# Performance work log

Hardware: AMD Instinct MI355X
Metric: run time of the kernel (lower is better)

Reference implementation:

```python
import jax, jax.numpy as jnp
import numpy as np

NUM_HEADS = 16

def setup_inputs() -> dict:
    key = jax.random.key(0)
    ks = jax.random.split(key, 7)
    B, Q, K, D = 4, 512, 4096, 1024
    return {
        'query':  jax.random.normal(ks[0], (B, Q, D), dtype=jnp.float32),
        'memory': jax.random.normal(ks[1], (B, K, D), dtype=jnp.float32),
        'bias':   jax.random.normal(ks[2], (B, K), dtype=jnp.float32),
        'Wq': jax.random.normal(ks[3], (D, D), dtype=jnp.float32) * (D ** -0.5),
        'Wk': jax.random.normal(ks[4], (D, D), dtype=jnp.float32) * (D ** -0.5),
        'Wv': jax.random.normal(ks[5], (D, D), dtype=jnp.float32) * (D ** -0.5),
        'Wo': jax.random.normal(ks[6], (D, D), dtype=jnp.float32) * (D ** -0.5),
    }

def reference(query, memory, bias, Wq, Wk, Wv, Wo):
    B, Qn, _ = query.shape
    _, Kn, _ = memory.shape
    H = NUM_HEADS
    E = Wq.shape[1]
    dh = E // H
    scale = dh ** -0.5
    # projections (bias-free linears), split heads: [B, H, len, dh]
    q = (query @ Wq).reshape(B, Qn, H, dh).transpose(0, 2, 1, 3)
    k = (memory @ Wk).reshape(B, Kn, H, dh).transpose(0, 2, 1, 3)
    v = (memory @ Wv).reshape(B, Kn, H, dh).transpose(0, 2, 1, 3)
    scores = jnp.einsum('bhqd,bhkd->bhqk', q, k) * scale
    scores = scores + bias[:, None, None, :]          # additive support bias over K
    weights = jax.nn.softmax(scores, axis=-1)          # dropout p=0.0 -> identity
    out = jnp.einsum('bhqk,bhkd->bhqd', weights, v)
    out = out.transpose(0, 2, 1, 3).reshape(B, Qn, E)
    return out @ Wo
```

## Files before the change

kernel.cpp:

```cpp
#include <hip/hip_runtime.h>

typedef __attribute__((ext_vector_type(8))) short bf16x8;
typedef __attribute__((ext_vector_type(4))) short bf16x4;
typedef __attribute__((ext_vector_type(4))) float f32x4;

#define MFMA32(a,b,c) __builtin_amdgcn_mfma_f32_16x16x32_bf16((a),(b),(c),0,0,0)
#define MFMA16(a,b,c) __builtin_amdgcn_mfma_f32_16x16x16bf16_1k((a),(b),(c),0,0,0)
#define LOG2E 1.44269504f

__device__ __forceinline__ unsigned short f2bf(float f) {
  unsigned int u = __float_as_uint(f);
  u += 0x7fffu + ((u >> 16) & 1u);
  return (unsigned short)(u >> 16);
}

__device__ __forceinline__ void cp16(const void* g, void* l) {
  __builtin_amdgcn_global_load_lds((const __attribute__((address_space(1))) void*)g,
                                   (__attribute__((address_space(3))) void*)l, 16, 0, 0);
}

__global__ void conv_both(const float* __restrict__ q, const float* __restrict__ m,
                          const float* __restrict__ bias,
                          unsigned short* __restrict__ qo, unsigned short* __restrict__ mo,
                          float* __restrict__ bz) {
  int i = blockIdx.x * 256 + threadIdx.x;
  if (i < 524288) {
    float4 v = ((const float4*)q)[i];
    ushort4 o; o.x = f2bf(v.x); o.y = f2bf(v.y); o.z = f2bf(v.z); o.w = f2bf(v.w);
    ((ushort4*)qo)[i] = o;
  } else if (i < 4718592) {
    int j = i - 524288;
    float4 v = ((const float4*)m)[j];
    ushort4 o; o.x = f2bf(v.x); o.y = f2bf(v.y); o.z = f2bf(v.z); o.w = f2bf(v.w);
    ((ushort4*)mo)[j] = o;
  } else {
    int j = i - 4718592;
    float4 v = ((const float4*)bias)[j];
    float4 o;
    o.x = __builtin_fmaf(v.x, LOG2E, -16.f);
    o.y = __builtin_fmaf(v.y, LOG2E, -16.f);
    o.z = __builtin_fmaf(v.z, LOG2E, -16.f);
    o.w = __builtin_fmaf(v.w, LOG2E, -16.f);
    ((float4*)bz)[j] = o;
  }
}

__global__ void transpose4(const float* __restrict__ Wq, const float* __restrict__ Wk,
                           const float* __restrict__ Wv, const float* __restrict__ Wo,
                           unsigned short* __restrict__ dst) {
  __shared__ float t[32][33];
  int z = blockIdx.z;
  const float* W = (z == 0) ? Wq : (z == 1) ? Wk : (z == 2) ? Wv : Wo;
  unsigned short* WT = dst + (size_t)z * 1048576;
  int bx = blockIdx.x * 32, by = blockIdx.y * 32;
  int x = threadIdx.x, y0 = threadIdx.y;
#pragma unroll
  for (int r = 0; r < 4; ++r)
    t[y0 + r * 8][x] = W[(size_t)(by + y0 + r * 8) * 1024 + bx + x];
  __syncthreads();
#pragma unroll
  for (int r = 0; r < 4; ++r)
    WT[(size_t)(bx + y0 + r * 8) * 1024 + by + x] = f2bf(t[x][y0 + r * 8]);
}

__global__ __launch_bounds__(256) void gemm_bt(
    const unsigned short* __restrict__ A, const unsigned short* __restrict__ B,
    float* __restrict__ Cf, unsigned short* __restrict__ Cb,
    int M, int N, int K, float scale)
{
  __shared__ __attribute__((aligned(16))) unsigned short lds[8192];
  int w = threadIdx.x >> 6, lane = threadIdx.x & 63;
  int lh = lane & 15, q4 = lane >> 4;
  int tm = blockIdx.y * 128, tn = blockIdx.x * 128;
  int wm = (w & 1) * 64, wn = (w >> 1) * 64;

  f32x4 acc[4][4] = {};

  for (int k0 = 0; k0 < K; k0 += 32) {
#pragma unroll
    for (int i = 0; i < 2; ++i) {
      int c = w * 2 + i;
      int o = c * 1024 + lane * 16;
      int row = o >> 6;
      int colu = (o & 63) >> 1;
      cp16(A + (size_t)(tm + row) * K + k0 + colu, lds + c * 512);
      cp16(B + (size_t)(tn + row) * K + k0 + colu, lds + 4096 + c * 512);
    }
    __syncthreads();
    bf16x8 afr[4], bfr[4];
#pragma unroll
    for (int r = 0; r < 4; ++r)
      afr[r] = *(const bf16x8*)(lds + (wm + r * 16 + lh) * 32 + q4 * 8);
#pragma unroll
    for (int c = 0; c < 4; ++c)
      bfr[c] = *(const bf16x8*)(lds + 4096 + (wn + c * 16 + lh) * 32 + q4 * 8);
#pragma unroll
    for (int r = 0; r < 4; ++r)
#pragma unroll
      for (int c = 0; c < 4; ++c)
        acc[r][c] = MFMA32(afr[r], bfr[c], acc[r][c]);
    __syncthreads();
  }

#pragma unroll
  for (int r = 0; r < 4; ++r)
#pragma unroll
    for (int c = 0; c < 4; ++c)
#pragma unroll
      for (int e = 0; e < 4; ++e) {
        int row = tm + wm + r * 16 + q4 * 4 + e;
        int col = tn + wn + c * 16 + lh;
        if (Cb) Cb[(size_t)row * N + col] = f2bf(acc[r][c][e] * scale);
        else    Cf[(size_t)row * N + col] = acc[r][c][e] * scale;
      }
}

__global__ __launch_bounds__(256) void gemm_bt64(
    const unsigned short* __restrict__ A, const unsigned short* __restrict__ B,
    float* __restrict__ Cf, unsigned short* __restrict__ Cb,
    int M, int N, int K, float scale)
{
  __shared__ __attribute__((aligned(16))) unsigned short lds[6144];
  int w = threadIdx.x >> 6, lane = threadIdx.x & 63;
  int lh = lane & 15, q4 = lane >> 4;
  int tm = blockIdx.y * 128, tn = blockIdx.x * 64;
  int wm = (w & 1) * 64, wn = (w >> 1) * 32;

  f32x4 acc[4][2] = {};

  for (int k0 = 0; k0 < K; k0 += 32) {
#pragma unroll
    for (int i = 0; i < 2; ++i) {
      int c = w * 2 + i;
      int o = c * 1024 + lane * 16;
      int row = o >> 6, colu = (o & 63) >> 1;
      cp16(A + (size_t)(tm + row) * K + k0 + colu, lds + c * 512);
    }
    {
      int o = w * 1024 + lane * 16;
      int row = o >> 6, colu = (o & 63) >> 1;
      cp16(B + (size_t)(tn + row) * K + k0 + colu, lds + 4096 + w * 512);
    }
    __syncthreads();
    bf16x8 afr[4], bfr[2];
#pragma unroll
    for (int r = 0; r < 4; ++r)
      afr[r] = *(const bf16x8*)(lds + (wm + r * 16 + lh) * 32 + q4 * 8);
#pragma unroll
    for (int c = 0; c < 2; ++c)
      bfr[c] = *(const bf16x8*)(lds + 4096 + (wn + c * 16 + lh) * 32 + q4 * 8);
#pragma unroll
    for (int r = 0; r < 4; ++r)
#pragma unroll
      for (int c = 0; c < 2; ++c)
        acc[r][c] = MFMA32(afr[r], bfr[c], acc[r][c]);
    __syncthreads();
  }

#pragma unroll
  for (int r = 0; r < 4; ++r)
#pragma unroll
    for (int c = 0; c < 2; ++c)
#pragma unroll
      for (int e = 0; e < 4; ++e) {
        int row = tm + wm + r * 16 + q4 * 4 + e;
        int col = tn + wn + c * 16 + lh;
        if (Cb) Cb[(size_t)row * N + col] = f2bf(acc[r][c][e] * scale);
        else    Cf[(size_t)row * N + col] = acc[r][c][e] * scale;
      }
}

__global__ __launch_bounds__(256) void attn_kernel(
    const unsigned short* __restrict__ Q, const unsigned short* __restrict__ Kp,
    const unsigned short* __restrict__ VT, const float* __restrict__ bz,
    float* __restrict__ po, float* __restrict__ lp)
{
  __shared__ __attribute__((aligned(16))) unsigned short Klds[4096];
  __shared__ __attribute__((aligned(16))) unsigned short Vlds[4096];
  int w = threadIdx.x >> 6, lane = threadIdx.x & 63;
  int lh = lane & 15, q4 = lane >> 4;

  int id = blockIdx.x;
  int xcd = id & 7, j = id >> 3;
  int ql = j & 7;
  int half = ql & 1, qt = ql >> 1;
  int bh = (j >> 3) * 8 + xcd;
  int b = bh >> 4, h = bh & 15;
  int q0 = qt * 128;
  int t00 = half * 2048;

  const unsigned short* Qb = Q + (size_t)(b * 512 + q0 + w * 32) * 1024 + h * 64;
  const unsigned short* Kb = Kp + (size_t)(b * 4096) * 1024 + h * 64;
  const unsigned short* Vb = VT + (size_t)(h * 64) * 16384 + b * 4096;
  const float* bzg = bz + (size_t)b * 4096;

  bf16x8 bq[2][2];
#pragma unroll
  for (int s = 0; s < 2; ++s)
#pragma unroll
    for (int th = 0; th < 2; ++th)
      bq[s][th] = *(const bf16x8*)(Qb + (size_t)(s * 16 + lh) * 1024 + th * 32 + q4 * 8);

  f32x4 oa[2][4] = {};
  float ls[2] = {0.f, 0.f};

  int rl = lane >> 3, blk = lane & 7;
  int sw = ((blk ^ rl) * 8);

  for (int ti = 0; ti < 32; ++ti) {
    int t = t00 + ti * 64;
#pragma unroll
    for (int r = 0; r < 2; ++r) {
      int seg = r * 4 + w;
      int row = seg * 8 + rl;
      cp16(Kb + (size_t)(t + row) * 1024 + sw, Klds + seg * 512);
      cp16(Vb + (size_t)row * 16384 + t + sw, Vlds + seg * 512);
    }
    __syncthreads();

    float4 bz4[4];
#pragma unroll
    for (int c = 0; c < 4; ++c)
      bz4[c] = *(const float4*)(bzg + t + c * 16 + q4 * 4);

    bf16x8 kf[4][2];
#pragma unroll
    for (int c = 0; c < 4; ++c)
#pragma unroll
      for (int th = 0; th < 2; ++th)
        kf[c][th] = *(const bf16x8*)(Klds + (c * 16 + lh) * 64 + (((th << 2) + q4) ^ (lh & 7)) * 8);
    bf16x4 vf[4][4];
#pragma unroll
    for (int c = 0; c < 4; ++c)
#pragma unroll
      for (int c2 = 0; c2 < 4; ++c2)
        vf[c][c2] = *(const bf16x4*)(Vlds + (c2 * 16 + lh) * 64 +
                                     (((c << 1) + (q4 >> 1)) ^ (lh & 7)) * 8 + (q4 & 1) * 4);

#pragma unroll
    for (int s = 0; s < 2; ++s) {
#pragma unroll
      for (int c = 0; c < 4; ++c) {
        f32x4 z = {};
        z = MFMA32(kf[c][0], bq[s][0], z);
        z = MFMA32(kf[c][1], bq[s][1], z);
        float bzf[4] = {bz4[c].x, bz4[c].y, bz4[c].z, bz4[c].w};
        bf16x4 pb;
        float ps = 0.f;
#pragma unroll
        for (int e = 0; e < 4; ++e) {
          float p = __builtin_amdgcn_exp2f(z[e] + bzf[e]);
          ps += p;
          pb[e] = (short)f2bf(p);
        }
        ls[s] += ps;
#pragma unroll
        for (int c2 = 0; c2 < 4; ++c2)
          oa[s][c2] = MFMA16(vf[c][c2], pb, oa[s][c2]);
      }
    }
    __syncthreads();
  }

#pragma unroll
  for (int s = 0; s < 2; ++s) {
    ls[s] += __shfl_xor(ls[s], 16);
    ls[s] += __shfl_xor(ls[s], 32);
  }

  int sl = bh * 4 + qt;
  float* pslice = po + (size_t)(half * 256 + sl) * 8192;
#pragma unroll
  for (int s = 0; s < 2; ++s) {
    if (q4 == 0) lp[half * 32768 + sl * 128 + w * 32 + s * 16 + lh] = ls[s];
#pragma unroll
    for (int c2 = 0; c2 < 4; ++c2)
#pragma unroll
      for (int e = 0; e < 4; ++e)
        pslice[(c2 * 16 + q4 * 4 + e) * 128 + w * 32 + s * 16 + lh] = oa[s][c2][e];
  }
}

__global__ void norm_kernel(const float* __restrict__ po, const float* __restrict__ lp,
                            unsigned short* __restrict__ ao) {
  int g = blockIdx.x * 256 + threadIdx.x;
  int d8 = (g & 7) * 8;
  int rowid = g >> 3;
  int bh = rowid >> 9, rq = rowid & 511, qt = rq >> 7, qcol = rq & 127;
  int sl = bh * 4 + qt;
  const float* p0 = po + (size_t)sl * 8192;
  const float* p1 = po + (size_t)(256 + sl) * 8192;
  float l = lp[sl * 128 + qcol] + lp[32768 + sl * 128 + qcol];
  float inv = 1.f / l;
  unsigned short o8[8];
#pragma unroll
  for (int k = 0; k < 8; ++k)
    o8[k] = f2bf((p0[(d8 + k) * 128 + qcol] + p1[(d8 + k) * 128 + qcol]) * inv);
  int b = bh >> 4, h = bh & 15;
  unsigned short* dst = ao + (size_t)(b * 512 + qt * 128 + qcol) * 1024 + h * 64 + d8;
  *(ushort4*)dst = *(ushort4*)o8;
  *(ushort4*)(dst + 4) = *(ushort4*)(o8 + 4);
}

extern "C" void kernel_launch(void* const* d_in, const int* in_sizes, int n_in,
                              void* d_out, int out_size, void* d_ws, size_t ws_size,
                              hipStream_t stream) {
  const float* query  = (const float*)d_in[0];
  const float* memory = (const float*)d_in[1];
  const float* bias   = (const float*)d_in[2];
  const float* Wq     = (const float*)d_in[3];
  const float* Wk     = (const float*)d_in[4];
  const float* Wv     = (const float*)d_in[5];
  const float* Wo     = (const float*)d_in[6];
  float* out = (float*)d_out;

  unsigned short* ws  = (unsigned short*)d_ws;
  unsigned short* qbf = ws;
  unsigned short* mbf = qbf + 2097152;
  unsigned short* WqT = mbf + 16777216;
  unsigned short* WkT = WqT + 1048576;
  unsigned short* WvT = WkT + 1048576;
  unsigned short* WoT = WvT + 1048576;
  unsigned short* qp  = WoT + 1048576;
  unsigned short* kp  = qp + 2097152;
  unsigned short* vT  = kp + 16777216;
  unsigned short* ao  = vT + 16777216;
  float* bzw = (float*)(ao + 2097152);
  float* po = (float*)ws;
  float* lp = po + 4194304;

  conv_both<<<18448, 256, 0, stream>>>(query, memory, bias, qbf, mbf, bzw);
  transpose4<<<dim3(32, 32, 4), dim3(32, 8), 0, stream>>>(Wq, Wk, Wv, Wo, WqT);

  gemm_bt64<<<dim3(16, 16), 256, 0, stream>>>(qbf, WqT, nullptr, qp, 2048, 1024, 1024, 0.125f * LOG2E);
  gemm_bt<<<dim3(8, 128), 256, 0, stream>>>(mbf, WkT, nullptr, kp, 16384, 1024, 1024, 1.f);
  gemm_bt<<<dim3(128, 8), 256, 0, stream>>>(WvT, mbf, nullptr, vT, 1024, 16384, 1024, 1.f);

  attn_kernel<<<512, 256, 0, stream>>>(qp, kp, vT, bzw, po, lp);
  norm_kernel<<<1024, 256, 0, stream>>>(po, lp, ao);

  gemm_bt64<<<dim3(16, 16), 256, 0, stream>>>(ao, WoT, out, nullptr, 2048, 1024, 1024, 1.f);
}
```

Before: 348.8 us.

## Fuse K and V projection GEMMs into one kernel sharing the memory tile

Replaces the two separate memory projection GEMMs with a single kernel that loads each memory tile once and multiplies it against both Wk^T and Wv^T, writing K in row-major order and V transposed with 4-element vector stores. This halves reads of the large memory activation and removes one launch. Block indices are remapped so consecutive blocks sharing an XCD work on the same M rows, improving L2 reuse. Doubling the accumulators raises register pressure, and launch_bounds(256,2) may force spills or cap occupancy.

After: 309.3 us. -11.3%, faster.

```diff
diff --git a/kernel.cpp b/kernel.cpp
--- a/kernel.cpp
+++ b/kernel.cpp
@@ -63,56 +63,68 @@
     WT[(size_t)(bx + y0 + r * 8) * 1024 + by + x] = f2bf(t[x][y0 + r * 8]);
 }
 
-__global__ __launch_bounds__(256) void gemm_bt(
-    const unsigned short* __restrict__ A, const unsigned short* __restrict__ B,
-    float* __restrict__ Cf, unsigned short* __restrict__ Cb,
-    int M, int N, int K, float scale)
+__global__ __launch_bounds__(256, 2) void gemm_kv(
+    const unsigned short* __restrict__ A,
+    const unsigned short* __restrict__ Bk,
+    const unsigned short* __restrict__ Bv,
+    unsigned short* __restrict__ Kp,
+    unsigned short* __restrict__ Vt)
 {
-  __shared__ __attribute__((aligned(16))) unsigned short lds[8192];
+  __shared__ __attribute__((aligned(16))) unsigned short lds[12288];
   int w = threadIdx.x >> 6, lane = threadIdx.x & 63;
   int lh = lane & 15, q4 = lane >> 4;
-  int tm = blockIdx.y * 128, tn = blockIdx.x * 128;
+  int id = blockIdx.x;
+  int xcd = id & 7, j = id >> 3;
+  int tm = (xcd * 16 + (j >> 3)) * 128;
+  int tn = (j & 7) * 128;
   int wm = (w & 1) * 64, wn = (w >> 1) * 64;
 
-  f32x4 acc[4][4] = {};
-
-  for (int k0 = 0; k0 < K; k0 += 32) {
+  f32x4 acck[4][4] = {}, accv[4][4] = {};
+
+  for (int k0 = 0; k0 < 1024; k0 += 32) {
 #pragma unroll
     for (int i = 0; i < 2; ++i) {
       int c = w * 2 + i;
       int o = c * 1024 + lane * 16;
-      int row = o >> 6;
-      int colu = (o & 63) >> 1;
-      cp16(A + (size_t)(tm + row) * K + k0 + colu, lds + c * 512);
-      cp16(B + (size_t)(tn + row) * K + k0 + colu, lds + 4096 + c * 512);
-    }
-    __syncthreads();
-    bf16x8 afr[4], bfr[4];
+      int row = o >> 6, colu = (o & 63) >> 1;
+      cp16(A  + (size_t)(tm + row) * 1024 + k0 + colu, lds + c * 512);
+      cp16(Bk + (size_t)(tn + row) * 1024 + k0 + colu, lds + 4096 + c * 512);
+      cp16(Bv + (size_t)(tn + row) * 1024 + k0 + colu, lds + 8192 + c * 512);
+    }
+    __syncthreads();
+    bf16x8 afr[4], bkf[4], bvf[4];
 #pragma unroll
     for (int r = 0; r < 4; ++r)
       afr[r] = *(const bf16x8*)(lds + (wm + r * 16 + lh) * 32 + q4 * 8);
 #pragma unroll
-    for (int c = 0; c < 4; ++c)
-      bfr[c] = *(const bf16x8*)(lds + 4096 + (wn + c * 16 + lh) * 32 + q4 * 8);
+    for (int c = 0; c < 4; ++c) {
+      bkf[c] = *(const bf16x8*)(lds + 4096 + (wn + c * 16 + lh) * 32 + q4 * 8);
+      bvf[c] = *(const bf16x8*)(lds + 8192 + (wn + c * 16 + lh) * 32 + q4 * 8);
+    }
 #pragma unroll
     for (int r = 0; r < 4; ++r)
 #pragma unroll
-      for (int c = 0; c < 4; ++c)
-        acc[r][c] = MFMA32(afr[r], bfr[c], acc[r][c]);
+      for (int c = 0; c < 4; ++c) {
+        acck[r][c] = MFMA32(afr[r], bkf[c], acck[r][c]);
+        accv[r][c] = MFMA32(afr[r], bvf[c], accv[r][c]);
+      }
     __syncthreads();
   }
 
 #pragma unroll
   for (int r = 0; r < 4; ++r)
 #pragma unroll
-    for (int c = 0; c < 4; ++c)
-#pragma unroll
-      for (int e = 0; e < 4; ++e) {
-        int row = tm + wm + r * 16 + q4 * 4 + e;
-        int col = tn + wn + c * 16 + lh;
-        if (Cb) Cb[(size_t)row * N + col] = f2bf(acc[r][c][e] * scale);
-        else    Cf[(size_t)row * N + col] = acc[r][c][e] * scale;
-      }
+    for (int c = 0; c < 4; ++c) {
+      int row = tm + wm + r * 16 + q4 * 4;
+      int col = tn + wn + c * 16 + lh;
+#pragma unroll
+      for (int e = 0; e < 4; ++e)
+        Kp[(size_t)(row + e) * 1024 + col] = f2bf(acck[r][c][e]);
+      ushort4 v4;
+      v4.x = f2bf(accv[r][c][0]); v4.y = f2bf(accv[r][c][1]);
+      v4.z = f2bf(accv[r][c][2]); v4.w = f2bf(accv[r][c][3]);
+      *(ushort4*)(Vt + (size_t)col * 16384 + row) = v4;
+    }
 }
 
 __global__ __launch_bounds__(256) void gemm_bt64(
@@ -333,8 +345,7 @@
   transpose4<<<dim3(32, 32, 4), dim3(32, 8), 0, stream>>>(Wq, Wk, Wv, Wo, WqT);
 
   gemm_bt64<<<dim3(16, 16), 256, 0, stream>>>(qbf, WqT, nullptr, qp, 2048, 1024, 1024, 0.125f * LOG2E);
-  gemm_bt<<<dim3(8, 128), 256, 0, stream>>>(mbf, WkT, nullptr, kp, 16384, 1024, 1024, 1.f);
-  gemm_bt<<<dim3(128, 8), 256, 0, stream>>>(WvT, mbf, nullptr, vT, 1024, 16384, 1024, 1.f);
+  gemm_kv<<<1024, 256, 0, stream>>>(mbf, WkT, WvT, kp, vT);
 
   attn_kernel<<<512, 256, 0, stream>>>(qp, kp, vT, bzw, po, lp);
   norm_kernel<<<1024, 256, 0, stream>>>(po, lp, ao);
```
